# Optimization experiments

Measured on AMD Instinct MI355X. Metric: run time of the kernel, lower is better.

## Reference

```python
import math
import jax, jax.numpy as jnp
import numpy as np

B, S, HID = 4, 2048, 1024
H, D = 16, 64  # num_head, head_dim
EPS = 1e-12  # F.normalize eps


def _qknorm(t, gamma):
    # t: [B, S, H, D]; F.normalize(dim=-1) * sqrt(D) * gamma[None]
    norm = jnp.sqrt(jnp.sum(t * t, axis=-1, keepdims=True))
    t = t / jnp.maximum(norm, EPS)
    return t * math.sqrt(D) * gamma  # gamma broadcasts over [B,S]


def setup_inputs() -> dict:
    key = jax.random.key(0)
    ks = jax.random.split(key, 8)
    s = 0.02
    return {
        "x": jax.random.normal(ks[0], (B, S, HID), jnp.float32),
        "q_w": jax.random.normal(ks[1], (HID, HID), jnp.float32) * s,
        "q_b": jnp.zeros((HID,), jnp.float32),
        "kv_w": jax.random.normal(ks[2], (2 * HID, HID), jnp.float32) * s,
        "kv_b": jnp.zeros((2 * HID,), jnp.float32),
        "gamma_q": jnp.ones((H, D), jnp.float32),
        "gamma_k": jnp.ones((H, D), jnp.float32),
        "out_w": jax.random.normal(ks[3], (HID, HID), jnp.float32) * s,
    }


def reference(x, q_w, q_b, kv_w, kv_b, gamma_q, gamma_k, out_w):
    # self-attention: context = x
    q = (x @ q_w.T + q_b).reshape(B, S, H, D)
    kv = x @ kv_w.T + kv_b  # [B, S, 2*HID]
    k, v = jnp.split(kv, 2, axis=-1)
    k = k.reshape(B, S, H, D)
    v = v.reshape(B, S, H, D)
    q = _qknorm(q, gamma_q)
    k = _qknorm(k, gamma_k)
    scores = jnp.einsum('bqhd,bkhd->bhqk', q, k)  # [B,H,S,S]
    attn = jax.nn.softmax(scores, axis=-1)
    out = jnp.einsum('bhqk,bkhd->bqhd', attn, v).reshape(B, S, HID)
    return out @ out_w.T
```

## Files before the change

### kernel.cpp

```cpp
#include <hip/hip_runtime.h>
#include <stdint.h>

#define B_ 4
#define S_ 2048
#define HID_ 1024
#define NH_ 16
#define HD_ 64

typedef __bf16 bf16x8 __attribute__((ext_vector_type(8)));
typedef __bf16 bf16x4 __attribute__((ext_vector_type(4)));
typedef float f32x4 __attribute__((ext_vector_type(4)));

__device__ inline void gload_lds16(const void* g, void* l) {
  __builtin_amdgcn_global_load_lds((const __attribute__((address_space(1))) unsigned int*)g,
                                   (__attribute__((address_space(3))) unsigned int*)l, 16, 0, 0);
}

__device__ inline f32x4 fmax4(f32x4 a, f32x4 b) {
  f32x4 r;
  r[0] = fmaxf(a[0], b[0]); r[1] = fmaxf(a[1], b[1]);
  r[2] = fmaxf(a[2], b[2]); r[3] = fmaxf(a[3], b[3]);
  return r;
}

__global__ __launch_bounds__(256) void cvt_bf16(const float* __restrict__ in, __bf16* __restrict__ out) {
  int i = (blockIdx.x * 256 + threadIdx.x) * 4;
  f32x4 v = *(const f32x4*)(in + i);
  bf16x4 o;
  o[0] = (__bf16)v[0]; o[1] = (__bf16)v[1]; o[2] = (__bf16)v[2]; o[3] = (__bf16)v[3];
  *(bf16x4*)(out + i) = o;
}

template <int MODE>
__global__ __launch_bounds__(256) void gemm_bt(const __bf16* __restrict__ A,
                                               const __bf16* __restrict__ Bt,
                                               const float* __restrict__ bias,
                                               const float* __restrict__ gamma,
                                               __bf16* __restrict__ Cb,
                                               float* __restrict__ Cf,
                                               __bf16* __restrict__ vt,
                                               int M, int N, int K) {
  const int n0 = blockIdx.x * 128;
  const int m0 = blockIdx.y * 128;
  const int tid  = threadIdx.x;
  const int wave = tid >> 6, lane = tid & 63;
  const int wm = wave >> 1, wn = wave & 1;
  const int lrow = lane & 15, lgrp = lane >> 4;

  __shared__ __bf16 sA[128][64];
  __shared__ __bf16 sB[128][64];

  f32x4 acc[4][4];
#pragma unroll
  for (int i = 0; i < 4; i++)
#pragma unroll
    for (int j = 0; j < 4; j++) acc[i][j] = f32x4{0.f, 0.f, 0.f, 0.f};

  for (int k0 = 0; k0 < K; k0 += 64) {
    __syncthreads();
#pragma unroll
    for (int c = 0; c < 4; c++) {
      const int row = wave * 32 + c * 8;
      const __bf16* ga = A + (size_t)(m0 + row + (lane >> 3)) * K + k0 + (lane & 7) * 8;
      gload_lds16(ga, &sA[row][0]);
      const __bf16* gb = Bt + (size_t)(n0 + row + (lane >> 3)) * K + k0 + (lane & 7) * 8;
      gload_lds16(gb, &sB[row][0]);
    }
    __syncthreads();
#pragma unroll
    for (int kk = 0; kk < 2; kk++) {
      bf16x8 af[4], bfr[4];
#pragma unroll
      for (int i = 0; i < 4; i++) {
        af[i]  = *(const bf16x8*)(&sA[wm * 64 + i * 16 + lrow][kk * 32 + 8 * lgrp]);
        bfr[i] = *(const bf16x8*)(&sB[wn * 64 + i * 16 + lrow][kk * 32 + 8 * lgrp]);
      }
#pragma unroll
      for (int i = 0; i < 4; i++)
#pragma unroll
        for (int j = 0; j < 4; j++)
          acc[i][j] = __builtin_amdgcn_mfma_f32_16x16x32_bf16(af[i], bfr[j], acc[i][j], 0, 0, 0);
    }
  }

  if (MODE != 1) {
    float bv[4];
#pragma unroll
    for (int j = 0; j < 4; j++) bv[j] = bias[n0 + wn * 64 + j * 16 + lrow];
#pragma unroll
    for (int i = 0; i < 4; i++)
#pragma unroll
      for (int j = 0; j < 4; j++)
#pragma unroll
        for (int r = 0; r < 4; r++) acc[i][j][r] += bv[j];
  }

  const bool do_norm = (MODE == 2) || (MODE == 3 && n0 < 1024);
  if (do_norm) {
    float g[4];
#pragma unroll
    for (int j = 0; j < 4; j++) g[j] = gamma[(n0 + wn * 64 + j * 16 + lrow) & 1023];
#pragma unroll
    for (int i = 0; i < 4; i++) {
#pragma unroll
      for (int r = 0; r < 4; r++) {
        float ss = acc[i][0][r] * acc[i][0][r] + acc[i][1][r] * acc[i][1][r] +
                   acc[i][2][r] * acc[i][2][r] + acc[i][3][r] * acc[i][3][r];
#pragma unroll
        for (int off = 1; off < 16; off <<= 1) ss += __shfl_xor(ss, off, 64);
        const float inv = 8.f / fmaxf(sqrtf(ss), 1e-12f);
        const int m = m0 + wm * 64 + i * 16 + lgrp * 4 + r;
#pragma unroll
        for (int j = 0; j < 4; j++) {
          const int n = (n0 + wn * 64 + j * 16 + lrow) & 1023;
          Cb[(size_t)m * 1024 + n] = (__bf16)(acc[i][j][r] * inv * g[j]);
        }
      }
    }
  } else if (MODE == 3) {
#pragma unroll
    for (int i = 0; i < 4; i++) {
#pragma unroll
      for (int j = 0; j < 4; j++) {
        const int nn = n0 + wn * 64 + j * 16 + lrow - 1024;
        const int h = nn >> 6, d = nn & 63;
        const int m = m0 + wm * 64 + i * 16 + lgrp * 4;
        const int b = m >> 11, s0 = m & 2047;
        bf16x4 pk;
#pragma unroll
        for (int r = 0; r < 4; r++) pk[r] = (__bf16)acc[i][j][r];
        *(bf16x4*)(vt + ((size_t)((b * 16 + h) * 64 + d)) * 2048 + s0) = pk;
      }
    }
  } else {
#pragma unroll
    for (int i = 0; i < 4; i++)
#pragma unroll
      for (int j = 0; j < 4; j++) {
        const int n = n0 + wn * 64 + j * 16 + lrow;
#pragma unroll
        for (int r = 0; r < 4; r++) {
          const int m = m0 + wm * 64 + i * 16 + lgrp * 4 + r;
          Cf[(size_t)m * N + n] = acc[i][j][r];
        }
      }
  }
}

__global__ __launch_bounds__(256) void attn_kernel(const __bf16* __restrict__ qm,
                                                   const __bf16* __restrict__ km,
                                                   const __bf16* __restrict__ vtm,
                                                   __bf16* __restrict__ o) {
  const int lin = blockIdx.y * gridDim.x + blockIdx.x;
  const int swz = (lin & 7) * 128 + (lin >> 3);
  const int qb = swz & 15;
  const int bh = swz >> 4;
  const int b = bh >> 4, h = bh & 15;
  const int q0 = qb * 128;
  const int tid = threadIdx.x, wave = tid >> 6, lane = tid & 63;
  const int lrow = lane & 15, lgrp = lane >> 4;

  __shared__ __bf16 sK[2][64 * 64];
  __shared__ __bf16 sVt[2][64 * 64];
  __shared__ __bf16 sP[4][16 * 64];

  const __bf16* kbase  = km + (size_t)(b * S_) * 1024 + h * 64;
  const __bf16* vtbase = vtm + (size_t)((b * 16 + h) * 64) * 2048;

  const int srow = lane >> 3;
  const int pchunk = lane & 7;

  auto stage = [&](int buf, int kt) {
#pragma unroll
    for (int i8 = 0; i8 < 2; ++i8) {
      const int rr = wave * 16 + i8 * 8;
      const int r = rr + srow;
      gload_lds16(kbase + (size_t)(kt * 64 + r) * 1024 + ((pchunk ^ (r & 7)) << 3),
                  &sK[buf][rr * 64]);
      gload_lds16(vtbase + (size_t)r * 2048 + kt * 64 + ((pchunk ^ (r & 7)) << 3),
                  &sVt[buf][rr * 64]);
    }
  };

  bf16x8 qf[2][2];
#pragma unroll
  for (int rt = 0; rt < 2; ++rt) {
    const __bf16* qp = qm + (size_t)(b * S_ + q0 + wave * 32 + rt * 16 + lrow) * 1024 + h * 64;
    qf[rt][0] = *(const bf16x8*)(qp + 8 * lgrp);
    qf[rt][1] = *(const bf16x8*)(qp + 32 + 8 * lgrp);
  }

  f32x4 accd[2][4];
#pragma unroll
  for (int rt = 0; rt < 2; ++rt)
#pragma unroll
    for (int dt = 0; dt < 4; ++dt) accd[rt][dt] = f32x4{0.f, 0.f, 0.f, 0.f};
  float m_r[2], l_r[2];
#pragma unroll
  for (int rt = 0; rt < 2; ++rt) { m_r[rt] = -1e30f; l_r[rt] = 0.f; }

  stage(0, 0);
  int buf = 0;
  for (int kt = 0; kt < S_ / 64; ++kt) {
    __syncthreads();
    if (kt + 1 < S_ / 64) stage(buf ^ 1, kt + 1);

    f32x4 sc[2][4];
#pragma unroll
    for (int rt = 0; rt < 2; ++rt)
#pragma unroll
      for (int t = 0; t < 4; ++t) sc[rt][t] = f32x4{0.f, 0.f, 0.f, 0.f};
#pragma unroll
    for (int t = 0; t < 4; ++t) {
      const int krow = t * 16 + lrow;
#pragma unroll
      for (int kk = 0; kk < 2; ++kk) {
        bf16x8 kf = *(const bf16x8*)(&sK[buf][krow * 64 + (((kk * 4 + lgrp) ^ (krow & 7)) << 3)]);
        sc[0][t] = __builtin_amdgcn_mfma_f32_16x16x32_bf16(kf, qf[0][kk], sc[0][t], 0, 0, 0);
        sc[1][t] = __builtin_amdgcn_mfma_f32_16x16x32_bf16(kf, qf[1][kk], sc[1][t], 0, 0, 0);
      }
    }

#pragma unroll
    for (int rt = 0; rt < 2; ++rt) {
      f32x4 mm = fmax4(fmax4(sc[rt][0], sc[rt][1]), fmax4(sc[rt][2], sc[rt][3]));
      float tm = fmaxf(fmaxf(mm[0], mm[1]), fmaxf(mm[2], mm[3]));
      tm = fmaxf(tm, __shfl_xor(tm, 16, 64));
      tm = fmaxf(tm, __shfl_xor(tm, 32, 64));
      const float mn = fmaxf(m_r[rt], tm);
      const float scl = __expf(m_r[rt] - mn);
      m_r[rt] = mn;

      float ps0 = 0.f, ps1 = 0.f;
#pragma unroll
      for (int t = 0; t < 4; ++t) {
        bf16x4 pk;
        float p0 = __expf(sc[rt][t][0] - mn);
        float p1 = __expf(sc[rt][t][1] - mn);
        float p2 = __expf(sc[rt][t][2] - mn);
        float p3 = __expf(sc[rt][t][3] - mn);
        ps0 += p0 + p2; ps1 += p1 + p3;
        pk[0] = (__bf16)p0; pk[1] = (__bf16)p1; pk[2] = (__bf16)p2; pk[3] = (__bf16)p3;
        *(bf16x4*)(&sP[wave][lrow * 64 + (((2 * t + (lgrp >> 1)) ^ (lrow & 7)) << 3) +
                             ((lgrp & 1) << 2)]) = pk;
      }
      float ps = ps0 + ps1;
      ps += __shfl_xor(ps, 16, 64);
      ps += __shfl_xor(ps, 32, 64);
      l_r[rt] = l_r[rt] * scl + ps;

      float sclr[4];
#pragma unroll
      for (int j = 0; j < 4; ++j) sclr[j] = __shfl(scl, lgrp * 4 + j, 64);
#pragma unroll
      for (int dt = 0; dt < 4; ++dt)
#pragma unroll
        for (int j = 0; j < 4; ++j) accd[rt][dt][j] *= sclr[j];

#pragma unroll
      for (int half = 0; half < 2; ++half) {
        bf16x8 pf = *(const bf16x8*)(&sP[wave][lrow * 64 + (((half * 4 + lgrp) ^ (lrow & 7)) << 3)]);
#pragma unroll
        for (int dt = 0; dt < 4; ++dt) {
          const int d = dt * 16 + lrow;
          bf16x8 vf = *(const bf16x8*)(&sVt[buf][d * 64 + (((half * 4 + lgrp) ^ (d & 7)) << 3)]);
          accd[rt][dt] = __builtin_amdgcn_mfma_f32_16x16x32_bf16(pf, vf, accd[rt][dt], 0, 0, 0);
        }
      }
    }
    buf ^= 1;
  }

#pragma unroll
  for (int rt = 0; rt < 2; ++rt) {
#pragma unroll
    for (int j = 0; j < 4; ++j) {
      const float lv = __shfl(l_r[rt], lgrp * 4 + j, 64);
      const float inv = 1.f / lv;
      const int row = b * S_ + q0 + wave * 32 + rt * 16 + lgrp * 4 + j;
      __bf16* ob = o + (size_t)row * 1024 + h * 64;
#pragma unroll
      for (int dt = 0; dt < 4; ++dt) ob[dt * 16 + lrow] = (__bf16)(accd[rt][dt][j] * inv);
    }
  }
}

extern "C" void kernel_launch(void* const* d_in, const int* in_sizes, int n_in,
                              void* d_out, int out_size, void* d_ws, size_t ws_size,
                              hipStream_t stream) {
  (void)in_sizes; (void)n_in; (void)out_size; (void)ws_size;
  const float* x       = (const float*)d_in[0];
  const float* q_w     = (const float*)d_in[1];
  const float* q_b     = (const float*)d_in[2];
  const float* kv_w    = (const float*)d_in[3];
  const float* kv_b    = (const float*)d_in[4];
  const float* gamma_q = (const float*)d_in[5];
  const float* gamma_k = (const float*)d_in[6];
  const float* out_w   = (const float*)d_in[7];
  float* out = (float*)d_out;

  char* ws = (char*)d_ws;
  __bf16* x_bf   = (__bf16*)(ws);
  __bf16* qw_bf  = (__bf16*)(ws + (16ull << 20));
  __bf16* kvw_bf = (__bf16*)(ws + (18ull << 20));
  __bf16* ow_bf  = (__bf16*)(ws + (22ull << 20));
  __bf16* q_bf   = (__bf16*)(ws + (24ull << 20));
  __bf16* k_bf   = (__bf16*)(ws + (40ull << 20));
  __bf16* vt_bf  = (__bf16*)(ws + (56ull << 20));
  __bf16* at_bf  = (__bf16*)(ws + (72ull << 20));

  cvt_bf16<<<8192, 256, 0, stream>>>(x, x_bf);
  cvt_bf16<<<1024, 256, 0, stream>>>(q_w, qw_bf);
  cvt_bf16<<<2048, 256, 0, stream>>>(kv_w, kvw_bf);
  cvt_bf16<<<1024, 256, 0, stream>>>(out_w, ow_bf);

  gemm_bt<2><<<dim3(8, 64), 256, 0, stream>>>(x_bf, qw_bf, q_b, gamma_q, q_bf, nullptr, nullptr,
                                              8192, 1024, 1024);
  gemm_bt<3><<<dim3(16, 64), 256, 0, stream>>>(x_bf, kvw_bf, kv_b, gamma_k, k_bf, nullptr, vt_bf,
                                               8192, 2048, 1024);

  attn_kernel<<<dim3(16, 64), 256, 0, stream>>>(q_bf, k_bf, vt_bf, at_bf);

  gemm_bt<1><<<dim3(8, 64), 256, 0, stream>>>(at_bf, ow_bf, nullptr, nullptr, nullptr, out, nullptr,
                                              8192, 1024, 1024);
}
```

Before: 370.5 us.

## Load K/V fragments directly from global memory and add lazy softmax rescaling

Drops the LDS double-buffered staging of K and V tiles and the per-tile __syncthreads. Each wave now reads its MFMA K and V fragments straight from global memory, relying on the L2/L1 caches for reuse across the four waves. Online softmax switches to exp2 with a folded log2e FMA and only rescales the accumulator and row sum when the running max grows by more than a threshold. This removes barrier and LDS traffic but makes every wave fetch K/V redundantly from global memory, which exposes load latency without explicit prefetch.

New measurement: 455.7 us. 23.0% more time.

```diff
diff --git a/kernel.cpp b/kernel.cpp
--- a/kernel.cpp
+++ b/kernel.cpp
@@ -151,6 +151,7 @@
                                                    const __bf16* __restrict__ km,
                                                    const __bf16* __restrict__ vtm,
                                                    __bf16* __restrict__ o) {
+  constexpr float LOG2E = 1.44269504f;
   const int lin = blockIdx.y * gridDim.x + blockIdx.x;
   const int swz = (lin & 7) * 128 + (lin >> 3);
   const int qb = swz & 15;
@@ -160,27 +161,10 @@
   const int tid = threadIdx.x, wave = tid >> 6, lane = tid & 63;
   const int lrow = lane & 15, lgrp = lane >> 4;
 
-  __shared__ __bf16 sK[2][64 * 64];
-  __shared__ __bf16 sVt[2][64 * 64];
   __shared__ __bf16 sP[4][16 * 64];
 
-  const __bf16* kbase  = km + (size_t)(b * S_) * 1024 + h * 64;
-  const __bf16* vtbase = vtm + (size_t)((b * 16 + h) * 64) * 2048;
-
-  const int srow = lane >> 3;
-  const int pchunk = lane & 7;
-
-  auto stage = [&](int buf, int kt) {
-#pragma unroll
-    for (int i8 = 0; i8 < 2; ++i8) {
-      const int rr = wave * 16 + i8 * 8;
-      const int r = rr + srow;
-      gload_lds16(kbase + (size_t)(kt * 64 + r) * 1024 + ((pchunk ^ (r & 7)) << 3),
-                  &sK[buf][rr * 64]);
-      gload_lds16(vtbase + (size_t)r * 2048 + kt * 64 + ((pchunk ^ (r & 7)) << 3),
-                  &sVt[buf][rr * 64]);
-    }
-  };
+  const __bf16* kbase  = km + (size_t)(b * S_) * 1024 + h * 64 + (size_t)lrow * 1024 + lgrp * 8;
+  const __bf16* vbase  = vtm + (size_t)((b * 16 + h) * 64) * 2048 + (size_t)lrow * 2048 + lgrp * 8;
 
   bf16x8 qf[2][2];
 #pragma unroll
@@ -195,15 +179,17 @@
   for (int rt = 0; rt < 2; ++rt)
 #pragma unroll
     for (int dt = 0; dt < 4; ++dt) accd[rt][dt] = f32x4{0.f, 0.f, 0.f, 0.f};
-  float m_r[2], l_r[2];
-#pragma unroll
-  for (int rt = 0; rt < 2; ++rt) { m_r[rt] = -1e30f; l_r[rt] = 0.f; }
-
-  stage(0, 0);
-  int buf = 0;
+  float m_r[2], m2_r[2], l_r[2];
+#pragma unroll
+  for (int rt = 0; rt < 2; ++rt) { m_r[rt] = -1e30f; m2_r[rt] = -1e30f; l_r[rt] = 0.f; }
+
   for (int kt = 0; kt < S_ / 64; ++kt) {
-    __syncthreads();
-    if (kt + 1 < S_ / 64) stage(buf ^ 1, kt + 1);
+    bf16x8 vfr[2][4];
+#pragma unroll
+    for (int half = 0; half < 2; ++half)
+#pragma unroll
+      for (int dt = 0; dt < 4; ++dt)
+        vfr[half][dt] = *(const bf16x8*)(vbase + (size_t)dt * 16 * 2048 + kt * 64 + half * 32);
 
     f32x4 sc[2][4];
 #pragma unroll
@@ -212,10 +198,9 @@
       for (int t = 0; t < 4; ++t) sc[rt][t] = f32x4{0.f, 0.f, 0.f, 0.f};
 #pragma unroll
     for (int t = 0; t < 4; ++t) {
-      const int krow = t * 16 + lrow;
 #pragma unroll
       for (int kk = 0; kk < 2; ++kk) {
-        bf16x8 kf = *(const bf16x8*)(&sK[buf][krow * 64 + (((kk * 4 + lgrp) ^ (krow & 7)) << 3)]);
+        bf16x8 kf = *(const bf16x8*)(kbase + (size_t)(kt * 64 + t * 16) * 1024 + kk * 32);
         sc[0][t] = __builtin_amdgcn_mfma_f32_16x16x32_bf16(kf, qf[0][kk], sc[0][t], 0, 0, 0);
         sc[1][t] = __builtin_amdgcn_mfma_f32_16x16x32_bf16(kf, qf[1][kk], sc[1][t], 0, 0, 0);
       }
@@ -227,18 +212,31 @@
       float tm = fmaxf(fmaxf(mm[0], mm[1]), fmaxf(mm[2], mm[3]));
       tm = fmaxf(tm, __shfl_xor(tm, 16, 64));
       tm = fmaxf(tm, __shfl_xor(tm, 32, 64));
-      const float mn = fmaxf(m_r[rt], tm);
-      const float scl = __expf(m_r[rt] - mn);
-      m_r[rt] = mn;
+
+      if (!__all(tm - m_r[rt] <= 8.0f)) {
+        const float mn = fmaxf(m_r[rt], tm);
+        const float scl = __builtin_exp2f((m_r[rt] - mn) * LOG2E);
+        m_r[rt] = mn;
+        m2_r[rt] = mn * LOG2E;
+        l_r[rt] *= scl;
+        float sclr[4];
+#pragma unroll
+        for (int j = 0; j < 4; ++j) sclr[j] = __shfl(scl, lgrp * 4 + j, 64);
+#pragma unroll
+        for (int dt = 0; dt < 4; ++dt)
+#pragma unroll
+          for (int j = 0; j < 4; ++j) accd[rt][dt][j] *= sclr[j];
+      }
 
       float ps0 = 0.f, ps1 = 0.f;
+      const float nm2 = -m2_r[rt];
 #pragma unroll
       for (int t = 0; t < 4; ++t) {
         bf16x4 pk;
-        float p0 = __expf(sc[rt][t][0] - mn);
-        float p1 = __expf(sc[rt][t][1] - mn);
-        float p2 = __expf(sc[rt][t][2] - mn);
-        float p3 = __expf(sc[rt][t][3] - mn);
+        const float p0 = __builtin_exp2f(fmaf(sc[rt][t][0], LOG2E, nm2));
+        const float p1 = __builtin_exp2f(fmaf(sc[rt][t][1], LOG2E, nm2));
+        const float p2 = __builtin_exp2f(fmaf(sc[rt][t][2], LOG2E, nm2));
+        const float p3 = __builtin_exp2f(fmaf(sc[rt][t][3], LOG2E, nm2));
         ps0 += p0 + p2; ps1 += p1 + p3;
         pk[0] = (__bf16)p0; pk[1] = (__bf16)p1; pk[2] = (__bf16)p2; pk[3] = (__bf16)p3;
         *(bf16x4*)(&sP[wave][lrow * 64 + (((2 * t + (lgrp >> 1)) ^ (lrow & 7)) << 3) +
@@ -247,28 +245,16 @@
       float ps = ps0 + ps1;
       ps += __shfl_xor(ps, 16, 64);
       ps += __shfl_xor(ps, 32, 64);
-      l_r[rt] = l_r[rt] * scl + ps;
-
-      float sclr[4];
-#pragma unroll
-      for (int j = 0; j < 4; ++j) sclr[j] = __shfl(scl, lgrp * 4 + j, 64);
-#pragma unroll
-      for (int dt = 0; dt < 4; ++dt)
-#pragma unroll
-        for (int j = 0; j < 4; ++j) accd[rt][dt][j] *= sclr[j];
+      l_r[rt] += ps;
 
 #pragma unroll
       for (int half = 0; half < 2; ++half) {
         bf16x8 pf = *(const bf16x8*)(&sP[wave][lrow * 64 + (((half * 4 + lgrp) ^ (lrow & 7)) << 3)]);
 #pragma unroll
-        for (int dt = 0; dt < 4; ++dt) {
-          const int d = dt * 16 + lrow;
-          bf16x8 vf = *(const bf16x8*)(&sVt[buf][d * 64 + (((half * 4 + lgrp) ^ (d & 7)) << 3)]);
-          accd[rt][dt] = __builtin_amdgcn_mfma_f32_16x16x32_bf16(pf, vf, accd[rt][dt], 0, 0, 0);
-        }
-      }
-    }
-    buf ^= 1;
+        for (int dt = 0; dt < 4; ++dt)
+          accd[rt][dt] = __builtin_amdgcn_mfma_f32_16x16x32_bf16(pf, vfr[half][dt], accd[rt][dt], 0, 0, 0);
+      }
+    }
   }
 
 #pragma unroll
```

## Use exp2 softmax with lazy rescaling and 512-thread attention blocks

Applied to the files above, without the earlier changes.

Folds log2(e) into the Q normalization scale so attention can use exp2 directly. Skips the running-max rescale of the accumulator unless some row's max grows by more than a threshold. Doubles the attention block to 8 waves covering 256 queries so each K/V tile staged in shared memory serves twice as many rows. It also reorders the PV MFMAs to reuse V fragments across both row tiles and raises wave priority around the MFMA sections. The lazy rescale depends on bounded score growth, which holds here because Q and K are normalized, and the larger block uses more registers and shared memory.

After: 344.2 us. 1.08x faster.

```diff
diff --git a/kernel.cpp b/kernel.cpp
--- a/kernel.cpp
+++ b/kernel.cpp
@@ -97,6 +97,7 @@
 
   const bool do_norm = (MODE == 2) || (MODE == 3 && n0 < 1024);
   if (do_norm) {
+    const float nscale = (MODE == 2) ? 8.f * 1.44269504f : 8.f;
     float g[4];
 #pragma unroll
     for (int j = 0; j < 4; j++) g[j] = gamma[(n0 + wn * 64 + j * 16 + lrow) & 1023];
@@ -108,7 +109,7 @@
                    acc[i][2][r] * acc[i][2][r] + acc[i][3][r] * acc[i][3][r];
 #pragma unroll
         for (int off = 1; off < 16; off <<= 1) ss += __shfl_xor(ss, off, 64);
-        const float inv = 8.f / fmaxf(sqrtf(ss), 1e-12f);
+        const float inv = nscale / fmaxf(sqrtf(ss), 1e-12f);
         const int m = m0 + wm * 64 + i * 16 + lgrp * 4 + r;
 #pragma unroll
         for (int j = 0; j < 4; j++) {
@@ -147,22 +148,23 @@
   }
 }
 
-__global__ __launch_bounds__(256) void attn_kernel(const __bf16* __restrict__ qm,
+__global__ __launch_bounds__(512) void attn_kernel(const __bf16* __restrict__ qm,
                                                    const __bf16* __restrict__ km,
                                                    const __bf16* __restrict__ vtm,
                                                    __bf16* __restrict__ o) {
+  constexpr float THR = 11.5416f;
   const int lin = blockIdx.y * gridDim.x + blockIdx.x;
-  const int swz = (lin & 7) * 128 + (lin >> 3);
-  const int qb = swz & 15;
-  const int bh = swz >> 4;
+  const int swz = (lin & 7) * 64 + (lin >> 3);
+  const int qb = swz & 7;
+  const int bh = swz >> 3;
   const int b = bh >> 4, h = bh & 15;
-  const int q0 = qb * 128;
+  const int q0 = qb * 256;
   const int tid = threadIdx.x, wave = tid >> 6, lane = tid & 63;
   const int lrow = lane & 15, lgrp = lane >> 4;
 
   __shared__ __bf16 sK[2][64 * 64];
   __shared__ __bf16 sVt[2][64 * 64];
-  __shared__ __bf16 sP[4][16 * 64];
+  __shared__ __bf16 sP[8][2][16 * 64];
 
   const __bf16* kbase  = km + (size_t)(b * S_) * 1024 + h * 64;
   const __bf16* vtbase = vtm + (size_t)((b * 16 + h) * 64) * 2048;
@@ -171,15 +173,12 @@
   const int pchunk = lane & 7;
 
   auto stage = [&](int buf, int kt) {
-#pragma unroll
-    for (int i8 = 0; i8 < 2; ++i8) {
-      const int rr = wave * 16 + i8 * 8;
-      const int r = rr + srow;
-      gload_lds16(kbase + (size_t)(kt * 64 + r) * 1024 + ((pchunk ^ (r & 7)) << 3),
-                  &sK[buf][rr * 64]);
-      gload_lds16(vtbase + (size_t)r * 2048 + kt * 64 + ((pchunk ^ (r & 7)) << 3),
-                  &sVt[buf][rr * 64]);
-    }
+    const int rr = wave * 8;
+    const int r = rr + srow;
+    gload_lds16(kbase + (size_t)(kt * 64 + r) * 1024 + ((pchunk ^ (r & 7)) << 3),
+                &sK[buf][rr * 64]);
+    gload_lds16(vtbase + (size_t)r * 2048 + kt * 64 + ((pchunk ^ (r & 7)) << 3),
+                &sVt[buf][rr * 64]);
   };
 
   bf16x8 qf[2][2];
@@ -210,6 +209,7 @@
     for (int rt = 0; rt < 2; ++rt)
 #pragma unroll
       for (int t = 0; t < 4; ++t) sc[rt][t] = f32x4{0.f, 0.f, 0.f, 0.f};
+    __builtin_amdgcn_s_setprio(1);
 #pragma unroll
     for (int t = 0; t < 4; ++t) {
       const int krow = t * 16 + lrow;
@@ -220,6 +220,7 @@
         sc[1][t] = __builtin_amdgcn_mfma_f32_16x16x32_bf16(kf, qf[1][kk], sc[1][t], 0, 0, 0);
       }
     }
+    __builtin_amdgcn_s_setprio(0);
 
 #pragma unroll
     for (int rt = 0; rt < 2; ++rt) {
@@ -227,47 +228,59 @@
       float tm = fmaxf(fmaxf(mm[0], mm[1]), fmaxf(mm[2], mm[3]));
       tm = fmaxf(tm, __shfl_xor(tm, 16, 64));
       tm = fmaxf(tm, __shfl_xor(tm, 32, 64));
-      const float mn = fmaxf(m_r[rt], tm);
-      const float scl = __expf(m_r[rt] - mn);
-      m_r[rt] = mn;
-
+
+      if (!__all(tm - m_r[rt] <= THR)) {
+        const float mn = fmaxf(m_r[rt], tm);
+        const float scl = __builtin_exp2f(m_r[rt] - mn);
+        m_r[rt] = mn;
+        l_r[rt] *= scl;
+        float sclr[4];
+#pragma unroll
+        for (int j = 0; j < 4; ++j) sclr[j] = __shfl(scl, lgrp * 4 + j, 64);
+#pragma unroll
+        for (int dt = 0; dt < 4; ++dt)
+#pragma unroll
+          for (int j = 0; j < 4; ++j) accd[rt][dt][j] *= sclr[j];
+      }
+
+      const float nm = m_r[rt];
       float ps0 = 0.f, ps1 = 0.f;
 #pragma unroll
       for (int t = 0; t < 4; ++t) {
         bf16x4 pk;
-        float p0 = __expf(sc[rt][t][0] - mn);
-        float p1 = __expf(sc[rt][t][1] - mn);
-        float p2 = __expf(sc[rt][t][2] - mn);
-        float p3 = __expf(sc[rt][t][3] - mn);
+        const float p0 = __builtin_exp2f(sc[rt][t][0] - nm);
+        const float p1 = __builtin_exp2f(sc[rt][t][1] - nm);
+        const float p2 = __builtin_exp2f(sc[rt][t][2] - nm);
+        const float p3 = __builtin_exp2f(sc[rt][t][3] - nm);
         ps0 += p0 + p2; ps1 += p1 + p3;
         pk[0] = (__bf16)p0; pk[1] = (__bf16)p1; pk[2] = (__bf16)p2; pk[3] = (__bf16)p3;
-        *(bf16x4*)(&sP[wave][lrow * 64 + (((2 * t + (lgrp >> 1)) ^ (lrow & 7)) << 3) +
-                             ((lgrp & 1) << 2)]) = pk;
+        *(bf16x4*)(&sP[wave][rt][lrow * 64 + (((2 * t + (lgrp >> 1)) ^ (lrow & 7)) << 3) +
+                                ((lgrp & 1) << 2)]) = pk;
       }
       float ps = ps0 + ps1;
       ps += __shfl_xor(ps, 16, 64);
       ps += __shfl_xor(ps, 32, 64);
-      l_r[rt] = l_r[rt] * scl + ps;
-
-      float sclr[4];
-#pragma unroll
-      for (int j = 0; j < 4; ++j) sclr[j] = __shfl(scl, lgrp * 4 + j, 64);
-#pragma unroll
-      for (int dt = 0; dt < 4; ++dt)
-#pragma unroll
-        for (int j = 0; j < 4; ++j) accd[rt][dt][j] *= sclr[j];
-
-#pragma unroll
-      for (int half = 0; half < 2; ++half) {
-        bf16x8 pf = *(const bf16x8*)(&sP[wave][lrow * 64 + (((half * 4 + lgrp) ^ (lrow & 7)) << 3)]);
-#pragma unroll
-        for (int dt = 0; dt < 4; ++dt) {
-          const int d = dt * 16 + lrow;
-          bf16x8 vf = *(const bf16x8*)(&sVt[buf][d * 64 + (((half * 4 + lgrp) ^ (d & 7)) << 3)]);
-          accd[rt][dt] = __builtin_amdgcn_mfma_f32_16x16x32_bf16(pf, vf, accd[rt][dt], 0, 0, 0);
-        }
-      }
-    }
+      l_r[rt] += ps;
+    }
+
+    __builtin_amdgcn_s_setprio(1);
+#pragma unroll
+    for (int half = 0; half < 2; ++half) {
+      bf16x8 vf[4];
+#pragma unroll
+      for (int dt = 0; dt < 4; ++dt) {
+        const int d = dt * 16 + lrow;
+        vf[dt] = *(const bf16x8*)(&sVt[buf][d * 64 + (((half * 4 + lgrp) ^ (lrow & 7)) << 3)]);
+      }
+#pragma unroll
+      for (int rt = 0; rt < 2; ++rt) {
+        bf16x8 pf = *(const bf16x8*)(&sP[wave][rt][lrow * 64 + (((half * 4 + lgrp) ^ (lrow & 7)) << 3)]);
+#pragma unroll
+        for (int dt = 0; dt < 4; ++dt)
+          accd[rt][dt] = __builtin_amdgcn_mfma_f32_16x16x32_bf16(pf, vf[dt], accd[rt][dt], 0, 0, 0);
+      }
+    }
+    __builtin_amdgcn_s_setprio(0);
     buf ^= 1;
   }
 
@@ -319,7 +332,7 @@
   gemm_bt<3><<<dim3(16, 64), 256, 0, stream>>>(x_bf, kvw_bf, kv_b, gamma_k, k_bf, nullptr, vt_bf,
                                                8192, 2048, 1024);
 
-  attn_kernel<<<dim3(16, 64), 256, 0, stream>>>(q_bf, k_bf, vt_bf, at_bf);
+  attn_kernel<<<dim3(8, 64), 512, 0, stream>>>(q_bf, k_bf, vt_bf, at_bf);
 
   gemm_bt<1><<<dim3(8, 64), 256, 0, stream>>>(at_bf, ow_bf, nullptr, nullptr, nullptr, out, nullptr,
                                               8192, 1024, 1024);
```
